# Optimization experiments

Hardware: AMD Instinct MI355X
Metric: run time of the kernel (lower is better)

Reference implementation:

```python
import jax, jax.numpy as jnp
import numpy as np

DRUG_DIM, PROT_DIM, HIDDEN_DIM, OUTPUT_DIM = 128, 128, 256, 256


def setup_inputs() -> dict:
    key = jax.random.key(0)
    ks = jax.random.split(key, 7)
    B, n_d, n_p = 8, 64, 1024
    s = lambda d: 1.0 / np.sqrt(d)
    return {
        "X_d": jax.random.normal(ks[0], (B, n_d, DRUG_DIM), dtype=jnp.float32),
        "X_p": jax.random.normal(ks[1], (B, n_p, PROT_DIM), dtype=jnp.float32),
        # nn.Linear(in, out) weights have shape (out, in); we store transposed (in, out)
        "W_d": jax.random.uniform(ks[2], (DRUG_DIM, HIDDEN_DIM), jnp.float32, -s(DRUG_DIM), s(DRUG_DIM)),
        "W_p": jax.random.uniform(ks[3], (PROT_DIM, HIDDEN_DIM), jnp.float32, -s(PROT_DIM), s(PROT_DIM)),
        "W_a": jax.random.uniform(ks[4], (DRUG_DIM, OUTPUT_DIM), jnp.float32, -s(DRUG_DIM), s(DRUG_DIM)),
        "W_b": jax.random.uniform(ks[5], (PROT_DIM, OUTPUT_DIM), jnp.float32, -s(PROT_DIM), s(PROT_DIM)),
        "w_score": jax.random.uniform(ks[6], (HIDDEN_DIM,), jnp.float32, -s(HIDDEN_DIM), s(HIDDEN_DIM)),
    }


def reference(X_d, X_p, W_d, W_p, W_a, W_b, w_score):
    # Projections: (B, n_d, H), (B, n_p, H), (B, n_d, O), (B, n_p, O)
    hd = jnp.einsum("bik,kh->bih", X_d, W_d)
    hp = jnp.einsum("bjk,kh->bjh", X_p, W_p)
    fd = jnp.einsum("bik,ko->bio", X_d, W_a)
    fp = jnp.einsum("bjk,ko->bjo", X_p, W_b)

    # N_ij = tanh(hd_i + hp_j): (B, n_d, n_p, H); scores = N @ w_score
    N = jnp.tanh(hd[:, :, None, :] + hp[:, None, :, :])
    scores = jnp.einsum("bijh,h->bij", N, w_score)
    A = jax.nn.softmax(scores, axis=-1)  # softmax over protein dim

    # f_ij = tanh(fd_i + fp_j): (B, n_d, n_p, O)
    f = jnp.tanh(fd[:, :, None, :] + fp[:, None, :, :])
    X_int = jnp.einsum("bij,bijo->bo", A, f)  # sum over i and j
    return X_int
```

## Files before the change

### kernel.cpp

```cpp
#include <hip/hip_runtime.h>

#define NB   8
#define ND   64
#define NP   1024
#define KDIM 128
#define HID  256
#define OUTD 256
#define CSC  2.885390081777927f

typedef __attribute__((ext_vector_type(8))) short  bf16x8;
typedef __attribute__((ext_vector_type(4))) float  f32x4;


__device__ __forceinline__ ushort f2bf(float f) {
    unsigned u = __float_as_uint(f);
    return (ushort)((u + 0x7FFFu + ((u >> 16) & 1u)) >> 16);
}

__global__ __launch_bounds__(256) void k_cast(
    const float* __restrict__ Xd, const float* __restrict__ Xp,
    const float* __restrict__ Wd, const float* __restrict__ Wa,
    const float* __restrict__ Wp, const float* __restrict__ Wb,
    ushort* __restrict__ Xdbf, ushort* __restrict__ Xpbf,
    ushort* __restrict__ WdT, ushort* __restrict__ WaT,
    ushort* __restrict__ WpT, ushort* __restrict__ WbT) {
    int blk = blockIdx.x, t = threadIdx.x;
    if (blk < 1024) {
        size_t i = ((size_t)blk << 10) + ((size_t)t << 2);
        float4 v = *(const float4*)(Xp + i);
        ushort4 o; o.x = f2bf(v.x); o.y = f2bf(v.y); o.z = f2bf(v.z); o.w = f2bf(v.w);
        *(ushort4*)(Xpbf + i) = o;
    } else if (blk < 1088) {
        size_t i = ((size_t)(blk - 1024) << 10) + ((size_t)t << 2);
        float4 v = *(const float4*)(Xd + i);
        ushort4 o; o.x = f2bf(v.x); o.y = f2bf(v.y); o.z = f2bf(v.z); o.w = f2bf(v.w);
        *(ushort4*)(Xdbf + i) = o;
    } else {
        int r = blk - 1088, mat = r >> 5;
        const float* W = (mat == 0) ? Wd : (mat == 1) ? Wa : (mat == 2) ? Wp : Wb;
        ushort* WT = (mat == 0) ? WdT : (mat == 1) ? WaT : (mat == 2) ? WpT : WbT;
        int o0 = ((r & 31) << 10) + (t << 2);
        int n = o0 >> 7, k0 = o0 & 127;
        ushort4 o;
        o.x = f2bf(W[(k0 + 0) * HID + n]);
        o.y = f2bf(W[(k0 + 1) * HID + n]);
        o.z = f2bf(W[(k0 + 2) * HID + n]);
        o.w = f2bf(W[(k0 + 3) * HID + n]);
        *(ushort4*)(WT + o0) = o;
    }
}

__global__ __launch_bounds__(256) void k_proj_mfma(
    const ushort* __restrict__ Xpbf, const ushort* __restrict__ Xdbf,
    const ushort* __restrict__ WdT, const ushort* __restrict__ WaT,
    const ushort* __restrict__ WpT, const ushort* __restrict__ WbT,
    float* __restrict__ Ehd, float* __restrict__ Efd,
    float* __restrict__ EhpT, float* __restrict__ Efp) {
    int blk = blockIdx.x, t = threadIdx.x;
    const ushort *A, *B;
    float* out; size_t obase; int ostride, am0, bn0;
    if (blk < 512) {
        int mt = blk >> 2, nt = blk & 3;
        A = Xpbf; am0 = mt * 64; B = WbT; bn0 = nt * 64;
        out = Efp; obase = (size_t)am0 * HID + bn0; ostride = HID;
    } else if (blk < 1024) {
        int r = blk - 512, b = r >> 6, rr = r & 63;
        int mt = rr >> 4, nt = rr & 15;
        A = WpT; am0 = mt * 64;
        B = Xpbf + (size_t)b * NP * KDIM; bn0 = nt * 64;
        out = EhpT; obase = ((size_t)(b * 256 + am0)) * NP + bn0; ostride = NP;
    } else if (blk < 1056) {
        int r = blk - 1024; int mt = r >> 2, nt = r & 3;
        A = Xdbf; am0 = mt * 64; B = WdT; bn0 = nt * 64;
        out = Ehd; obase = (size_t)am0 * HID + bn0; ostride = HID;
    } else {
        int r = blk - 1056; int mt = r >> 2, nt = r & 3;
        A = Xdbf; am0 = mt * 64; B = WaT; bn0 = nt * 64;
        out = Efd; obase = (size_t)am0 * HID + bn0; ostride = HID;
    }
    int l = t & 63, w = t >> 6;
    int wm = (w >> 1) << 5, wn = (w & 1) << 5;
    int lr = l & 15, lk = (l >> 4) << 3;
    const ushort* Ab = A + (size_t)(am0 + wm + lr) * KDIM + lk;
    const ushort* Bb = B + (size_t)(bn0 + wn + lr) * KDIM + lk;

    bf16x8 af[2][4], bfr[2][4];
#pragma unroll
    for (int f = 0; f < 2; ++f)
#pragma unroll
        for (int ks = 0; ks < 4; ++ks) {
            af[f][ks]  = *(const bf16x8*)(Ab + (size_t)(f << 4) * KDIM + (ks << 5));
            bfr[f][ks] = *(const bf16x8*)(Bb + (size_t)(f << 4) * KDIM + (ks << 5));
        }

    f32x4 acc[2][2];
#pragma unroll
    for (int mf = 0; mf < 2; ++mf)
#pragma unroll
        for (int nf = 0; nf < 2; ++nf) acc[mf][nf] = (f32x4){0.f, 0.f, 0.f, 0.f};
#pragma unroll
    for (int ks = 0; ks < 4; ++ks)
#pragma unroll
        for (int mf = 0; mf < 2; ++mf)
#pragma unroll
            for (int nf = 0; nf < 2; ++nf)
                acc[mf][nf] = __builtin_amdgcn_mfma_f32_16x16x32_bf16(
                    af[mf][ks], bfr[nf][ks], acc[mf][nf], 0, 0, 0);

#pragma unroll
    for (int mf = 0; mf < 2; ++mf)
#pragma unroll
        for (int nf = 0; nf < 2; ++nf)
#pragma unroll
            for (int r = 0; r < 4; ++r) {
                int m = wm + (mf << 4) + ((l >> 4) << 2) + r;
                int n = wn + (nf << 4) + (l & 15);
                out[obase + (size_t)m * ostride + n] =
                    __builtin_amdgcn_exp2f(acc[mf][nf][r] * CSC);
            }
}

__global__ __launch_bounds__(1024) void k_fused(
    const float* __restrict__ Ehd, const float* __restrict__ EhpT,
    const float* __restrict__ Efd, const float* __restrict__ Efp,
    const float* __restrict__ wsc, float* __restrict__ part) {
    int blk = blockIdx.x;
    int b = blk & 7, pair = blk >> 3;
    int row0 = b * ND + pair * 2;
    int t = threadIdx.x;

    __shared__ float2 hrow[256];
    __shared__ float  w2s[256];
    __shared__ float2 a2[1024];
    __shared__ float  sred[8 * 1024];
    __shared__ float  wsum0[16], wsum1[16];

    if (t < 256) {
        hrow[t] = make_float2(Ehd[((size_t)row0 << 8) + t],
                              Ehd[((size_t)(row0 + 1) << 8) + t]);
        w2s[t] = -2.0f * wsc[t];
    }
    __syncthreads();

    {
        int jq = t & 255, hq = t >> 8;
        const float* pB = EhpT + ((size_t)((b << 8) + (hq << 6))) * NP + (jq << 2);
        float a00 = 0, a01 = 0, a02 = 0, a03 = 0;
        float a10 = 0, a11 = 0, a12 = 0, a13 = 0;
        for (int hh = 0; hh < 64; ++hh) {
            int h = (hq << 6) + hh;
            float2 hv = hrow[h];
            float wv = w2s[h];
            float4 p = *(const float4*)(pB + (size_t)hh * NP);
            a00 = fmaf(wv, __builtin_amdgcn_rcpf(fmaf(hv.x, p.x, 1.f)), a00);
            a01 = fmaf(wv, __builtin_amdgcn_rcpf(fmaf(hv.x, p.y, 1.f)), a01);
            a02 = fmaf(wv, __builtin_amdgcn_rcpf(fmaf(hv.x, p.z, 1.f)), a02);
            a03 = fmaf(wv, __builtin_amdgcn_rcpf(fmaf(hv.x, p.w, 1.f)), a03);
            a10 = fmaf(wv, __builtin_amdgcn_rcpf(fmaf(hv.y, p.x, 1.f)), a10);
            a11 = fmaf(wv, __builtin_amdgcn_rcpf(fmaf(hv.y, p.y, 1.f)), a11);
            a12 = fmaf(wv, __builtin_amdgcn_rcpf(fmaf(hv.y, p.z, 1.f)), a12);
            a13 = fmaf(wv, __builtin_amdgcn_rcpf(fmaf(hv.y, p.w, 1.f)), a13);
        }
        int base = (hq << 8) + jq;
        sred[0 * 1024 + base] = a00;  sred[1 * 1024 + base] = a01;
        sred[2 * 1024 + base] = a02;  sred[3 * 1024 + base] = a03;
        sred[4 * 1024 + base] = a10;  sred[5 * 1024 + base] = a11;
        sred[6 * 1024 + base] = a12;  sred[7 * 1024 + base] = a13;
    }
    __syncthreads();

    {
        int jq2 = t >> 2, c = t & 3;
        const float* p0 = sred + c * 1024 + jq2;
        const float* p1 = sred + (4 + c) * 1024 + jq2;
        float sc0 = (p0[0] + p0[256]) + (p0[512] + p0[768]);
        float sc1 = (p1[0] + p1[256]) + (p1[512] + p1[768]);
        const float L2E = 1.4426950408889634f;
        float e0 = __builtin_amdgcn_exp2f(sc0 * L2E);
        float e1 = __builtin_amdgcn_exp2f(sc1 * L2E);
        float s0 = e0, s1 = e1;
#pragma unroll
        for (int off = 32; off > 0; off >>= 1) {
            s0 += __shfl_xor(s0, off, 64);
            s1 += __shfl_xor(s1, off, 64);
        }
        if ((t & 63) == 0) { wsum0[t >> 6] = s0; wsum1[t >> 6] = s1; }
        __syncthreads();
        float tot0 = 0.f, tot1 = 0.f;
#pragma unroll
        for (int w = 0; w < 16; ++w) { tot0 += wsum0[w]; tot1 += wsum1[w]; }
        float sn0 = -2.0f * __builtin_amdgcn_rcpf(tot0);
        float sn1 = -2.0f * __builtin_amdgcn_rcpf(tot1);
        a2[t] = make_float2(e0 * sn0, e1 * sn1);
    }
    __syncthreads();

    {
        int oq = t & 63, jg = t >> 6;
        int o0 = oq << 2;
        float4 fd0 = *(const float4*)(Efd + ((size_t)row0 << 8) + o0);
        float4 fd1 = *(const float4*)(Efd + ((size_t)(row0 + 1) << 8) + o0);
        const float* fpB = Efp + ((size_t)(b * NP + (jg << 6)) << 8) + o0;
        float b00 = 0, b01 = 0, b02 = 0, b03 = 0;
        float b10 = 0, b11 = 0, b12 = 0, b13 = 0;
        for (int jj = 0; jj < 64; ++jj) {
            float4 f = *(const float4*)(fpB + ((size_t)jj << 8));
            float2 av = a2[(jg << 6) + jj];
            b00 = fmaf(av.x, __builtin_amdgcn_rcpf(fmaf(fd0.x, f.x, 1.f)), b00);
            b01 = fmaf(av.x, __builtin_amdgcn_rcpf(fmaf(fd0.y, f.y, 1.f)), b01);
            b02 = fmaf(av.x, __builtin_amdgcn_rcpf(fmaf(fd0.z, f.z, 1.f)), b02);
            b03 = fmaf(av.x, __builtin_amdgcn_rcpf(fmaf(fd0.w, f.w, 1.f)), b03);
            b10 = fmaf(av.y, __builtin_amdgcn_rcpf(fmaf(fd1.x, f.x, 1.f)), b10);
            b11 = fmaf(av.y, __builtin_amdgcn_rcpf(fmaf(fd1.y, f.y, 1.f)), b11);
            b12 = fmaf(av.y, __builtin_amdgcn_rcpf(fmaf(fd1.z, f.z, 1.f)), b12);
            b13 = fmaf(av.y, __builtin_amdgcn_rcpf(fmaf(fd1.w, f.w, 1.f)), b13);
        }
        __syncthreads();
        int base = (jg << 6) + oq;
        sred[0 * 1024 + base] = b00;  sred[1 * 1024 + base] = b01;
        sred[2 * 1024 + base] = b02;  sred[3 * 1024 + base] = b03;
        sred[4 * 1024 + base] = b10;  sred[5 * 1024 + base] = b11;
        sred[6 * 1024 + base] = b12;  sred[7 * 1024 + base] = b13;
    }
    __syncthreads();

    if (t < 512) {
        int r = t >> 8, o = t & 255;
        int oq2 = o >> 2, c2 = o & 3;
        const float* pk = sred + (r * 4 + c2) * 1024 + oq2;
        float s = 0.f;
#pragma unroll
        for (int g = 0; g < 16; ++g) s += pk[g << 6];
        part[((size_t)((b << 6) + (pair << 1) + r) << 8) + o] = s;
    }
}

__global__ __launch_bounds__(256) void k_reduce(
    const float* __restrict__ part, float* __restrict__ out) {
    int b = blockIdx.x, t = threadIdx.x;
    float s = 64.0f;
#pragma unroll 8
    for (int i = 0; i < 64; ++i)
        s += part[((size_t)((b << 6) + i) << 8) + t];
    out[(b << 8) + t] = s;
}

extern "C" void kernel_launch(void* const* d_in, const int* in_sizes, int n_in,
                              void* d_out, int out_size, void* d_ws, size_t ws_size,
                              hipStream_t stream) {
    const float* Xd  = (const float*)d_in[0];
    const float* Xp  = (const float*)d_in[1];
    const float* Wd  = (const float*)d_in[2];
    const float* Wp  = (const float*)d_in[3];
    const float* Wa  = (const float*)d_in[4];
    const float* Wb  = (const float*)d_in[5];
    const float* wsc = (const float*)d_in[6];
    float* out = (float*)d_out;

    float* ws = (float*)d_ws;
    float* Ehd  = ws;
    float* Efd  = Ehd + NB * ND * HID;
    float* EhpT = Efd + NB * ND * OUTD;
    float* Efp  = EhpT + NB * NP * HID;
    float* stage = Efp + NB * NP * OUTD;
    ushort* Xpbf = (ushort*)stage;
    ushort* Xdbf = Xpbf + NB * NP * KDIM;
    ushort* WdT  = Xdbf + 65536;
    ushort* WaT  = WdT + 32768;
    ushort* WpT  = WaT + 32768;
    ushort* WbT  = WpT + 32768;
    float* part  = stage;

    k_cast     <<<1216, 256, 0, stream>>>(Xd, Xp, Wd, Wa, Wp, Wb,
                                          Xdbf, Xpbf, WdT, WaT, WpT, WbT);
    k_proj_mfma<<<1088, 256, 0, stream>>>(Xpbf, Xdbf, WdT, WaT, WpT, WbT,
                                          Ehd, Efd, EhpT, Efp);
    k_fused    <<<256, 1024, 0, stream>>>(Ehd, EhpT, Efd, Efp, wsc, part);
    k_reduce   <<<NB, 256, 0, stream>>>(part, out);
}
```

Measured before the change: 65.70 us.

## Split fused attention kernel over protein quarters with deferred softmax normalization

Splits the protein dimension of the fused kernel into four chunks, giving 1024 blocks of 512 threads instead of 256 blocks of 1024 threads, for better occupancy and load balance across CUs. Each block writes an unnormalized numerator and a partial softmax denominator. The reduce kernel combines the four chunks and divides per drug row, so no max subtraction or global-sum sync is needed inside a block. Shared-memory reduction arrays use a padded stride. The cost is extra global traffic for the partials and more serial work in the small reduce kernel.

```diff
diff --git a/kernel.cpp b/kernel.cpp
--- a/kernel.cpp
+++ b/kernel.cpp
@@ -7,6 +7,7 @@
 #define HID  256
 #define OUTD 256
 #define CSC  2.885390081777927f
+#define PSTR 520
 
 typedef __attribute__((ext_vector_type(8))) short  bf16x8;
 typedef __attribute__((ext_vector_type(4))) float  f32x4;
@@ -120,20 +121,21 @@
             }
 }
 
-__global__ __launch_bounds__(1024) void k_fused(
+__global__ __launch_bounds__(512, 8) void k_fused(
     const float* __restrict__ Ehd, const float* __restrict__ EhpT,
     const float* __restrict__ Efd, const float* __restrict__ Efp,
-    const float* __restrict__ wsc, float* __restrict__ part) {
+    const float* __restrict__ wsc, float* __restrict__ num,
+    float* __restrict__ den) {
     int blk = blockIdx.x;
-    int b = blk & 7, pair = blk >> 3;
+    int b = blk & 7, pair = (blk >> 3) & 31, jh = blk >> 8;
     int row0 = b * ND + pair * 2;
     int t = threadIdx.x;
 
     __shared__ float2 hrow[256];
     __shared__ float  w2s[256];
-    __shared__ float2 a2[1024];
-    __shared__ float  sred[8 * 1024];
-    __shared__ float  wsum0[16], wsum1[16];
+    __shared__ float2 a2[256];
+    __shared__ float  sred[8 * PSTR];
+    __shared__ float  wsum0[4], wsum1[4];
 
     if (t < 256) {
         hrow[t] = make_float2(Ehd[((size_t)row0 << 8) + t],
@@ -143,12 +145,13 @@
     __syncthreads();
 
     {
-        int jq = t & 255, hq = t >> 8;
-        const float* pB = EhpT + ((size_t)((b << 8) + (hq << 6))) * NP + (jq << 2);
+        int jq = t & 63, hq = t >> 6;
+        const float* pB = EhpT + ((size_t)((b << 8) + (hq << 5))) * NP
+                        + (jh << 8) + (jq << 2);
         float a00 = 0, a01 = 0, a02 = 0, a03 = 0;
         float a10 = 0, a11 = 0, a12 = 0, a13 = 0;
-        for (int hh = 0; hh < 64; ++hh) {
-            int h = (hq << 6) + hh;
+        for (int hh = 0; hh < 32; ++hh) {
+            int h = (hq << 5) + hh;
             float2 hv = hrow[h];
             float wv = w2s[h];
             float4 p = *(const float4*)(pB + (size_t)hh * NP);
@@ -161,51 +164,55 @@
             a12 = fmaf(wv, __builtin_amdgcn_rcpf(fmaf(hv.y, p.z, 1.f)), a12);
             a13 = fmaf(wv, __builtin_amdgcn_rcpf(fmaf(hv.y, p.w, 1.f)), a13);
         }
-        int base = (hq << 8) + jq;
-        sred[0 * 1024 + base] = a00;  sred[1 * 1024 + base] = a01;
-        sred[2 * 1024 + base] = a02;  sred[3 * 1024 + base] = a03;
-        sred[4 * 1024 + base] = a10;  sred[5 * 1024 + base] = a11;
-        sred[6 * 1024 + base] = a12;  sred[7 * 1024 + base] = a13;
-    }
-    __syncthreads();
-
-    {
-        int jq2 = t >> 2, c = t & 3;
-        const float* p0 = sred + c * 1024 + jq2;
-        const float* p1 = sred + (4 + c) * 1024 + jq2;
-        float sc0 = (p0[0] + p0[256]) + (p0[512] + p0[768]);
-        float sc1 = (p1[0] + p1[256]) + (p1[512] + p1[768]);
+        int base = (hq << 6) + jq;
+        sred[0 * PSTR + base] = a00;  sred[1 * PSTR + base] = a01;
+        sred[2 * PSTR + base] = a02;  sred[3 * PSTR + base] = a03;
+        sred[4 * PSTR + base] = a10;  sred[5 * PSTR + base] = a11;
+        sred[6 * PSTR + base] = a12;  sred[7 * PSTR + base] = a13;
+    }
+    __syncthreads();
+
+    if (t < 256) {
+        int jq2 = t >> 2, joff = t & 3;
+        const float* p0 = sred + joff * PSTR + jq2;
+        const float* p1 = sred + (4 + joff) * PSTR + jq2;
+        float sc0 = 0.f, sc1 = 0.f;
+#pragma unroll
+        for (int hq = 0; hq < 8; ++hq) {
+            sc0 += p0[hq << 6];
+            sc1 += p1[hq << 6];
+        }
         const float L2E = 1.4426950408889634f;
-        float e0 = __builtin_amdgcn_exp2f(sc0 * L2E);
-        float e1 = __builtin_amdgcn_exp2f(sc1 * L2E);
-        float s0 = e0, s1 = e1;
+        float u0 = __builtin_amdgcn_exp2f(sc0 * L2E);
+        float u1 = __builtin_amdgcn_exp2f(sc1 * L2E);
+        a2[t] = make_float2(-2.f * u0, -2.f * u1);
+        float s0 = u0, s1 = u1;
 #pragma unroll
         for (int off = 32; off > 0; off >>= 1) {
             s0 += __shfl_xor(s0, off, 64);
             s1 += __shfl_xor(s1, off, 64);
         }
         if ((t & 63) == 0) { wsum0[t >> 6] = s0; wsum1[t >> 6] = s1; }
-        __syncthreads();
-        float tot0 = 0.f, tot1 = 0.f;
-#pragma unroll
-        for (int w = 0; w < 16; ++w) { tot0 += wsum0[w]; tot1 += wsum1[w]; }
-        float sn0 = -2.0f * __builtin_amdgcn_rcpf(tot0);
-        float sn1 = -2.0f * __builtin_amdgcn_rcpf(tot1);
-        a2[t] = make_float2(e0 * sn0, e1 * sn1);
-    }
-    __syncthreads();
+    }
+    __syncthreads();
+    if (t == 0) {
+        den[((size_t)row0 << 2) + jh] =
+            (wsum0[0] + wsum0[1]) + (wsum0[2] + wsum0[3]);
+        den[((size_t)(row0 + 1) << 2) + jh] =
+            (wsum1[0] + wsum1[1]) + (wsum1[2] + wsum1[3]);
+    }
 
     {
         int oq = t & 63, jg = t >> 6;
         int o0 = oq << 2;
         float4 fd0 = *(const float4*)(Efd + ((size_t)row0 << 8) + o0);
         float4 fd1 = *(const float4*)(Efd + ((size_t)(row0 + 1) << 8) + o0);
-        const float* fpB = Efp + ((size_t)(b * NP + (jg << 6)) << 8) + o0;
+        const float* fpB = Efp + ((size_t)(b * NP + (jh << 8) + (jg << 5)) << 8) + o0;
         float b00 = 0, b01 = 0, b02 = 0, b03 = 0;
         float b10 = 0, b11 = 0, b12 = 0, b13 = 0;
-        for (int jj = 0; jj < 64; ++jj) {
+        for (int jj = 0; jj < 32; ++jj) {
             float4 f = *(const float4*)(fpB + ((size_t)jj << 8));
-            float2 av = a2[(jg << 6) + jj];
+            float2 av = a2[(jg << 5) + jj];
             b00 = fmaf(av.x, __builtin_amdgcn_rcpf(fmaf(fd0.x, f.x, 1.f)), b00);
             b01 = fmaf(av.x, __builtin_amdgcn_rcpf(fmaf(fd0.y, f.y, 1.f)), b01);
             b02 = fmaf(av.x, __builtin_amdgcn_rcpf(fmaf(fd0.z, f.z, 1.f)), b02);
@@ -217,31 +224,36 @@
         }
         __syncthreads();
         int base = (jg << 6) + oq;
-        sred[0 * 1024 + base] = b00;  sred[1 * 1024 + base] = b01;
-        sred[2 * 1024 + base] = b02;  sred[3 * 1024 + base] = b03;
-        sred[4 * 1024 + base] = b10;  sred[5 * 1024 + base] = b11;
-        sred[6 * 1024 + base] = b12;  sred[7 * 1024 + base] = b13;
-    }
-    __syncthreads();
-
-    if (t < 512) {
+        sred[0 * PSTR + base] = b00;  sred[1 * PSTR + base] = b01;
+        sred[2 * PSTR + base] = b02;  sred[3 * PSTR + base] = b03;
+        sred[4 * PSTR + base] = b10;  sred[5 * PSTR + base] = b11;
+        sred[6 * PSTR + base] = b12;  sred[7 * PSTR + base] = b13;
+    }
+    __syncthreads();
+
+    {
         int r = t >> 8, o = t & 255;
-        int oq2 = o >> 2, c2 = o & 3;
-        const float* pk = sred + (r * 4 + c2) * 1024 + oq2;
+        const float* pk = sred + ((r << 2) + (o & 3)) * PSTR + (o >> 2);
         float s = 0.f;
 #pragma unroll
-        for (int g = 0; g < 16; ++g) s += pk[g << 6];
-        part[((size_t)((b << 6) + (pair << 1) + r) << 8) + o] = s;
+        for (int g = 0; g < 8; ++g) s += pk[g << 6];
+        num[(((size_t)(row0 + r) << 2) + jh) * 256 + o] = s;
     }
 }
 
 __global__ __launch_bounds__(256) void k_reduce(
-    const float* __restrict__ part, float* __restrict__ out) {
+    const float* __restrict__ num, const float* __restrict__ den,
+    float* __restrict__ out) {
     int b = blockIdx.x, t = threadIdx.x;
     float s = 64.0f;
-#pragma unroll 8
-    for (int i = 0; i < 64; ++i)
-        s += part[((size_t)((b << 6) + i) << 8) + t];
+    for (int i = 0; i < 64; ++i) {
+        size_t row = (size_t)(b * 64 + i);
+        float D = (den[(row << 2) + 0] + den[(row << 2) + 1]) +
+                  (den[(row << 2) + 2] + den[(row << 2) + 3]);
+        const float* nb = num + (row << 2) * 256 + t;
+        float n = (nb[0] + nb[256]) + (nb[512] + nb[768]);
+        s += n * __builtin_amdgcn_rcpf(D);
+    }
     out[(b << 8) + t] = s;
 }
 
@@ -269,12 +281,13 @@
     ushort* WaT  = WdT + 32768;
     ushort* WpT  = WaT + 32768;
     ushort* WbT  = WpT + 32768;
-    float* part  = stage;
+    float* numb = stage + 622592;
+    float* denb = numb + 524288;
 
     k_cast     <<<1216, 256, 0, stream>>>(Xd, Xp, Wd, Wa, Wp, Wb,
                                           Xdbf, Xpbf, WdT, WaT, WpT, WbT);
     k_proj_mfma<<<1088, 256, 0, stream>>>(Xpbf, Xdbf, WdT, WaT, WpT, WbT,
                                           Ehd, Efd, EhpT, Efp);
-    k_fused    <<<256, 1024, 0, stream>>>(Ehd, EhpT, Efd, Efp, wsc, part);
-    k_reduce   <<<NB, 256, 0, stream>>>(part, out);
-}
+    k_fused    <<<1024, 512, 0, stream>>>(Ehd, EhpT, Efd, Efp, wsc, numb, denb);
+    k_reduce   <<<NB, 256, 0, stream>>>(numb, denb, out);
+}
```

Result: no change. 64.96 us (-1.1%).
